# Kernel optimization log

Measured on AMD Instinct MI355X. Metric: run time of the kernel, lower is better.

The kernel has to match this reference:

```python
import jax, jax.numpy as jnp
import numpy as np

B, S, D = 32, 2048, 1024
E, K = 64, 8
N_TAGS = 128


def setup_inputs() -> dict:
    key = jax.random.key(0)
    k1, k2, k3, k4, k5, k6 = jax.random.split(key, 6)
    hidden_states = jax.random.normal(k1, (B, S, D), dtype=jnp.float32)
    subw_indices = jax.random.randint(k2, (B, E, K), 0, S, dtype=jnp.int32)
    subw_counts = jax.random.randint(k3, (B, E), 1, K + 1, dtype=jnp.int32)
    num_entities = jax.random.randint(k4, (B,), 1, E + 1, dtype=jnp.int32)
    fc_w = jax.random.normal(k5, (N_TAGS, D), dtype=jnp.float32) * (1.0 / np.sqrt(D))
    fc_b = jax.random.normal(k6, (N_TAGS,), dtype=jnp.float32) * 0.01
    return {
        "hidden_states": hidden_states,
        "subw_indices": subw_indices,
        "subw_counts": subw_counts,
        "num_entities": num_entities,
        "fc_w": fc_w,
        "fc_b": fc_b,
    }


def reference(hidden_states, subw_indices, subw_counts, num_entities, fc_w, fc_b):
    # Gather subword embeddings: [B, E, K, D]
    flat_idx = subw_indices.reshape(B, E * K)                      # [B, E*K]
    gathered = jnp.take_along_axis(
        hidden_states, flat_idx[:, :, None], axis=1
    ).reshape(B, E, K, D)
    # Mask padded subword slots and mean-pool per entity
    subw_mask = (jnp.arange(K)[None, None, :] < subw_counts[:, :, None])  # [B,E,K]
    subw_mask = subw_mask.astype(hidden_states.dtype)
    ent_emb = jnp.einsum("bekd,bek->bed", gathered, subw_mask)
    ent_emb = ent_emb / subw_counts[:, :, None].astype(hidden_states.dtype)
    # Zero-pad entities past num_entities (original pads with zero_emb)
    ent_mask = (jnp.arange(E)[None, :] < num_entities[:, None])    # [B,E]
    ent_emb = ent_emb * ent_mask[:, :, None].astype(hidden_states.dtype)
    # fc applied to all positions (padded rows yield the bias, as in original)
    logits = jnp.einsum("bed,td->bet", ent_emb, fc_w) + fc_b
    return logits
```

## Files before the change

### kernel.cpp

```cpp
#include <hip/hip_runtime.h>

#define BB 32
#define SS 2048
#define DD 1024
#define EE 64
#define KK 8
#define TT 128
#define MM (BB * EE)

#define KSPLIT 8
#define KCHUNK (DD / KSPLIT)
#define MT 32
#define LSTR 136

typedef __attribute__((ext_vector_type(8))) short short8;
typedef __attribute__((ext_vector_type(4))) float f32x4;

__device__ __forceinline__ unsigned short f2bf(float f) {
    union { float f; unsigned int u; } v; v.f = f;
    unsigned int u = v.u + 0x7FFFu + ((v.u >> 16) & 1u);
    return (unsigned short)(u >> 16);
}

__global__ __launch_bounds__(256) void fc_fused_kernel(
    const float* __restrict__ hs,
    const int*   __restrict__ subw_idx,
    const int*   __restrict__ subw_cnt,
    const int*   __restrict__ num_ent,
    const float* __restrict__ fc_w,
    float* __restrict__ part)
{
    __shared__ unsigned short As[MT][LSTR];
    __shared__ unsigned short Bs[TT][LSTR];

    const int bx = blockIdx.x;
    const int mt = bx >> 3;
    const int ks = bx & (KSPLIT - 1);
    const int t  = threadIdx.x;
    const int wid  = t >> 6;
    const int lane = t & 63;
    const int k0 = ks * KCHUNK;

    {
        const int r   = t >> 3;
        const int sub = t & 7;
        const int be  = mt * MT + r;
        const int b   = be >> 6;
        const int e   = be & 63;
        const int cnt = subw_cnt[be];
        const int ne  = num_ent[b];
        const float scale = (e < ne) ? (1.0f / (float)cnt) : 0.0f;
        const int* idxp = subw_idx + (size_t)be * KK;

        float acc[16];
        #pragma unroll
        for (int j = 0; j < 16; ++j) acc[j] = 0.f;

        for (int k = 0; k < cnt; ++k) {
            const int s = idxp[k];
            const float4* p = (const float4*)(hs + ((size_t)b * SS + s) * DD
                                              + k0 + sub * 16);
            #pragma unroll
            for (int j = 0; j < 4; ++j) {
                float4 v = p[j];
                acc[4*j+0] += v.x; acc[4*j+1] += v.y;
                acc[4*j+2] += v.z; acc[4*j+3] += v.w;
            }
        }
        ushort4 o[4];
        #pragma unroll
        for (int j = 0; j < 4; ++j) {
            o[j].x = f2bf(acc[4*j+0] * scale);
            o[j].y = f2bf(acc[4*j+1] * scale);
            o[j].z = f2bf(acc[4*j+2] * scale);
            o[j].w = f2bf(acc[4*j+3] * scale);
        }
        *(ushort4*)&As[r][sub * 16 + 0]  = o[0];
        *(ushort4*)&As[r][sub * 16 + 4]  = o[1];
        *(ushort4*)&As[r][sub * 16 + 8]  = o[2];
        *(ushort4*)&As[r][sub * 16 + 12] = o[3];
    }

    {
        const int n = t >> 1;
        const int h = (t & 1) * 64;
        const float4* wrow = (const float4*)(fc_w + (size_t)n * DD + k0 + h);
        #pragma unroll
        for (int j = 0; j < 16; ++j) {
            float4 v = wrow[j];
            ushort4 o;
            o.x = f2bf(v.x); o.y = f2bf(v.y); o.z = f2bf(v.z); o.w = f2bf(v.w);
            *(ushort4*)&Bs[n][h + j * 4] = o;
        }
    }
    __syncthreads();

    const int msub  = (wid & 1) * 16;
    const int nbase = (wid >> 1) * 64;
    const int lm = lane & 15;
    const int lq = (lane >> 4) * 8;

    f32x4 acc0 = {0.f,0.f,0.f,0.f}, acc1 = {0.f,0.f,0.f,0.f};
    f32x4 acc2 = {0.f,0.f,0.f,0.f}, acc3 = {0.f,0.f,0.f,0.f};

    #pragma unroll
    for (int kstep = 0; kstep < KCHUNK / 32; ++kstep) {
        const int kc = kstep * 32 + lq;
        short8 a  = *(const short8*)&As[msub + lm][kc];
        short8 b0 = *(const short8*)&Bs[nbase +  0 + lm][kc];
        short8 b1 = *(const short8*)&Bs[nbase + 16 + lm][kc];
        short8 b2 = *(const short8*)&Bs[nbase + 32 + lm][kc];
        short8 b3 = *(const short8*)&Bs[nbase + 48 + lm][kc];
        acc0 = __builtin_amdgcn_mfma_f32_16x16x32_bf16(a, b0, acc0, 0, 0, 0);
        acc1 = __builtin_amdgcn_mfma_f32_16x16x32_bf16(a, b1, acc1, 0, 0, 0);
        acc2 = __builtin_amdgcn_mfma_f32_16x16x32_bf16(a, b2, acc2, 0, 0, 0);
        acc3 = __builtin_amdgcn_mfma_f32_16x16x32_bf16(a, b3, acc3, 0, 0, 0);
    }

    float* outp = part + (size_t)ks * MM * TT;
    const int mrow = mt * MT + msub + (lane >> 4) * 4;
    const int ncol = nbase + (lane & 15);
    #pragma unroll
    for (int r = 0; r < 4; ++r) {
        const size_t base = (size_t)(mrow + r) * TT + ncol;
        outp[base +  0] = acc0[r];
        outp[base + 16] = acc1[r];
        outp[base + 32] = acc2[r];
        outp[base + 48] = acc3[r];
    }
}

__global__ __launch_bounds__(256) void reduce_kernel(
    const float* __restrict__ part,
    const float* __restrict__ fc_b,
    float* __restrict__ out)
{
    const int i = blockIdx.x * 256 + threadIdx.x;
    float4 s = *(const float4*)(fc_b + (i & 31) * 4);
    #pragma unroll
    for (int k = 0; k < KSPLIT; ++k) {
        float4 p = *(const float4*)(part + (size_t)k * MM * TT + 4 * (size_t)i);
        s.x += p.x; s.y += p.y; s.z += p.z; s.w += p.w;
    }
    *(float4*)(out + 4 * (size_t)i) = s;
}

extern "C" void kernel_launch(void* const* d_in, const int* in_sizes, int n_in,
                              void* d_out, int out_size, void* d_ws, size_t ws_size,
                              hipStream_t stream) {
    const float* hs       = (const float*)d_in[0];
    const int*   subw_idx = (const int*)  d_in[1];
    const int*   subw_cnt = (const int*)  d_in[2];
    const int*   num_ent  = (const int*)  d_in[3];
    const float* fc_w     = (const float*)d_in[4];
    const float* fc_b     = (const float*)d_in[5];
    float*       out      = (float*)d_out;
    float*       part     = (float*)d_ws;

    fc_fused_kernel<<<(MM / MT) * KSPLIT, 256, 0, stream>>>(
        hs, subw_idx, subw_cnt, num_ent, fc_w, part);
    reduce_kernel<<<(MM * TT / 4) / 256, 256, 0, stream>>>(part, fc_b, out);
}
```

Before: 319.9 us.

## Replace split-K partial buffer with atomic adds and batch gather loads

The split-K partial-sum buffer and separate reduce kernel are replaced by a bias-init kernel followed by float atomicAdd of each K-chunk's MFMA result directly into the output. The subword gather now loads all eight indices with vector loads and issues four rows of loads at a time, with masked FMAs, so more memory requests are in flight. This removes the write and reread of eight partial output copies, at the cost of atomic contention, nondeterministic summation order, and loading padded subword rows that a shorter loop would have skipped.

```diff
diff --git a/kernel.cpp b/kernel.cpp
--- a/kernel.cpp
+++ b/kernel.cpp
@@ -22,13 +22,22 @@
     return (unsigned short)(u >> 16);
 }
 
+__global__ __launch_bounds__(256) void bias_init_kernel(
+    const float* __restrict__ fc_b,
+    float* __restrict__ out)
+{
+    const int i = blockIdx.x * 256 + threadIdx.x;
+    float4 b = *(const float4*)(fc_b + (i & 31) * 4);
+    *(float4*)(out + 4 * (size_t)i) = b;
+}
+
 __global__ __launch_bounds__(256) void fc_fused_kernel(
     const float* __restrict__ hs,
     const int*   __restrict__ subw_idx,
     const int*   __restrict__ subw_cnt,
     const int*   __restrict__ num_ent,
     const float* __restrict__ fc_w,
-    float* __restrict__ part)
+    float* __restrict__ out)
 {
     __shared__ unsigned short As[MT][LSTR];
     __shared__ unsigned short Bs[TT][LSTR];
@@ -50,23 +59,41 @@
         const int cnt = subw_cnt[be];
         const int ne  = num_ent[b];
         const float scale = (e < ne) ? (1.0f / (float)cnt) : 0.0f;
-        const int* idxp = subw_idx + (size_t)be * KK;
+
+        const int4* ip = (const int4*)(subw_idx + (size_t)be * KK);
+        const int4 i0 = ip[0];
+        const int4 i1 = ip[1];
+        int idx[8] = { i0.x, i0.y, i0.z, i0.w, i1.x, i1.y, i1.z, i1.w };
+
+        const float* base = hs + (size_t)b * SS * DD + k0 + sub * 16;
 
         float acc[16];
         #pragma unroll
         for (int j = 0; j < 16; ++j) acc[j] = 0.f;
 
-        for (int k = 0; k < cnt; ++k) {
-            const int s = idxp[k];
-            const float4* p = (const float4*)(hs + ((size_t)b * SS + s) * DD
-                                              + k0 + sub * 16);
+        #pragma unroll
+        for (int half = 0; half < 2; ++half) {
+            float4 v[4][4];
             #pragma unroll
-            for (int j = 0; j < 4; ++j) {
-                float4 v = p[j];
-                acc[4*j+0] += v.x; acc[4*j+1] += v.y;
-                acc[4*j+2] += v.z; acc[4*j+3] += v.w;
+            for (int k = 0; k < 4; ++k) {
+                const int kk = half * 4 + k;
+                const int s = (kk < cnt) ? idx[kk] : idx[0];
+                const float4* p = (const float4*)(base + (size_t)s * DD);
+                v[k][0] = p[0]; v[k][1] = p[1]; v[k][2] = p[2]; v[k][3] = p[3];
+            }
+            #pragma unroll
+            for (int k = 0; k < 4; ++k) {
+                const float w = ((half * 4 + k) < cnt) ? 1.0f : 0.0f;
+                #pragma unroll
+                for (int j = 0; j < 4; ++j) {
+                    acc[4*j+0] = fmaf(w, v[k][j].x, acc[4*j+0]);
+                    acc[4*j+1] = fmaf(w, v[k][j].y, acc[4*j+1]);
+                    acc[4*j+2] = fmaf(w, v[k][j].z, acc[4*j+2]);
+                    acc[4*j+3] = fmaf(w, v[k][j].w, acc[4*j+3]);
+                }
             }
         }
+
         ushort4 o[4];
         #pragma unroll
         for (int j = 0; j < 4; ++j) {
@@ -117,32 +144,16 @@
         acc3 = __builtin_amdgcn_mfma_f32_16x16x32_bf16(a, b3, acc3, 0, 0, 0);
     }
 
-    float* outp = part + (size_t)ks * MM * TT;
     const int mrow = mt * MT + msub + (lane >> 4) * 4;
     const int ncol = nbase + (lane & 15);
     #pragma unroll
     for (int r = 0; r < 4; ++r) {
         const size_t base = (size_t)(mrow + r) * TT + ncol;
-        outp[base +  0] = acc0[r];
-        outp[base + 16] = acc1[r];
-        outp[base + 32] = acc2[r];
-        outp[base + 48] = acc3[r];
+        atomicAdd(out + base +  0, acc0[r]);
+        atomicAdd(out + base + 16, acc1[r]);
+        atomicAdd(out + base + 32, acc2[r]);
+        atomicAdd(out + base + 48, acc3[r]);
     }
-}
-
-__global__ __launch_bounds__(256) void reduce_kernel(
-    const float* __restrict__ part,
-    const float* __restrict__ fc_b,
-    float* __restrict__ out)
-{
-    const int i = blockIdx.x * 256 + threadIdx.x;
-    float4 s = *(const float4*)(fc_b + (i & 31) * 4);
-    #pragma unroll
-    for (int k = 0; k < KSPLIT; ++k) {
-        float4 p = *(const float4*)(part + (size_t)k * MM * TT + 4 * (size_t)i);
-        s.x += p.x; s.y += p.y; s.z += p.z; s.w += p.w;
-    }
-    *(float4*)(out + 4 * (size_t)i) = s;
 }
 
 extern "C" void kernel_launch(void* const* d_in, const int* in_sizes, int n_in,
@@ -155,9 +166,8 @@
     const float* fc_w     = (const float*)d_in[4];
     const float* fc_b     = (const float*)d_in[5];
     float*       out      = (float*)d_out;
-    float*       part     = (float*)d_ws;
 
+    bias_init_kernel<<<(MM * TT / 4) / 256, 256, 0, stream>>>(fc_b, out);
     fc_fused_kernel<<<(MM / MT) * KSPLIT, 256, 0, stream>>>(
-        hs, subw_idx, subw_cnt, num_ent, fc_w, part);
-    reduce_kernel<<<(MM * TT / 4) / 256, 256, 0, stream>>>(part, fc_b, out);
+        hs, subw_idx, subw_cnt, num_ent, fc_w, out);
 }
```

After: 319.4 us. No clear change (-0.1%).
